# Performance work log

Measured on AMD Instinct MI355X. Metric: run time of the kernel, lower is better.

Reference implementation:

```python
import jax, jax.numpy as jnp
import numpy as np

B, L, DIM, H, D = 2, 2048, 1024, 16, 64


def setup_inputs() -> dict:
    key = jax.random.key(0)
    ks = jax.random.split(key, 20)
    s = 1.0 / np.sqrt(DIM)
    inp = {
        "query": jax.random.normal(ks[0], (B, L, DIM), jnp.float32),
        "keys": jax.random.normal(ks[1], (B, L, DIM), jnp.float32),
        "values": jax.random.normal(ks[2], (B, L, DIM), jnp.float32),
        "focus_vector": jax.random.normal(ks[3], (B, DIM), jnp.float32),
        "temporal_weights": jax.random.normal(ks[4], (B, L), jnp.float32),
        "importance_weights": jax.random.normal(ks[5], (B, L), jnp.float32),
        # linear params, stored [in, out] for x @ W + b
        "Wq": jax.random.normal(ks[6], (DIM, H * D), jnp.float32) * s,
        "bq": jnp.zeros((H * D,), jnp.float32),
        "Wk": jax.random.normal(ks[7], (DIM, H * D), jnp.float32) * s,
        "bk": jnp.zeros((H * D,), jnp.float32),
        "Wv": jax.random.normal(ks[8], (DIM, H * D), jnp.float32) * s,
        "bv": jnp.zeros((H * D,), jnp.float32),
        "Wp": jax.random.normal(ks[9], (H * D, DIM), jnp.float32) * s,
        "bp": jnp.zeros((DIM,), jnp.float32),
        "Wt": jax.random.normal(ks[10], (DIM, 1), jnp.float32) * s,
        "bt": jnp.zeros((1,), jnp.float32),
        "Wi": jax.random.normal(ks[11], (DIM, 1), jnp.float32) * s,
        "bi": jnp.zeros((1,), jnp.float32),
    }
    return inp


def reference(query, keys, values, focus_vector, temporal_weights, importance_weights,
              Wq, bq, Wk, bk, Wv, bv, Wp, bp, Wt, bt, Wi, bi):
    b, l, _ = query.shape
    # QKV projections -> [B, H, L, D]
    q = (query @ Wq + bq).reshape(b, l, H, D).transpose(0, 2, 1, 3)
    k = (keys @ Wk + bk).reshape(b, -1, H, D).transpose(0, 2, 1, 3)
    v = (values @ Wv + bv).reshape(b, -1, H, D).transpose(0, 2, 1, 3)
    scores = jnp.einsum("bhqd,bhkd->bhqk", q, k) / np.sqrt(D).astype(np.float32)
    # gate-modulated weights over keys [B, Lk]
    temporal_scores = (keys @ Wt + bt)[..., 0]
    tw = jax.nn.softmax(temporal_scores * temporal_weights, axis=-1)
    importance_scores = (keys @ Wi + bi)[..., 0]
    iw = jax.nn.softmax(importance_scores * importance_weights, axis=-1)
    rw = jax.nn.softmax(jnp.einsum("bkd,bd->bk", keys, focus_vector), axis=-1)
    combined = (tw + iw + rw) / 3.0
    scores = scores * combined[:, None, None, :]
    weights = jax.nn.softmax(scores, axis=-1)  # dropout is identity in eval
    out = jnp.einsum("bhqk,bhkd->bhqd", weights, v)
    out = out.transpose(0, 2, 1, 3).reshape(b, l, H * D)
    out = out @ Wp + bp
    return out, weights
```

## Files before the change

kernel.cpp:

```cpp
#include <hip/hip_runtime.h>
#include <hip/hip_bf16.h>
#include <cstdint>

#define DEV static __device__ __forceinline__

typedef __attribute__((ext_vector_type(8))) short short8_;
typedef __attribute__((ext_vector_type(4))) float float4_;
typedef __attribute__((ext_vector_type(4))) float f4v;
typedef __attribute__((ext_vector_type(4))) unsigned short u16x4;
typedef __attribute__((ext_vector_type(2))) uint32_t u32x2;
typedef unsigned short u16;

constexpr int Bb   = 2;
constexpr int Ls   = 2048;
constexpr int DIMc = 1024;
constexpr int Hh   = 16;
constexpr int Dd   = 64;
constexpr int BL   = Bb * Ls;
constexpr int HD   = Hh * Dd;

DEV u16 f2bf(float f) {
  union { float f; uint32_t u; } v; v.f = f;
  return (u16)((v.u + 0x7fffu + ((v.u >> 16) & 1u)) >> 16);
}

DEV float4_ mfma16(short8_ a, short8_ b, float4_ c) {
  return __builtin_amdgcn_mfma_f32_16x16x32_bf16(a, b, c, 0, 0, 0);
}

DEV void gload_lds16(const void* g, void* l) {
  __builtin_amdgcn_global_load_lds(
      (const __attribute__((address_space(1))) void*)g,
      (__attribute__((address_space(3))) void*)l, 16, 0, 0);
}

__global__ void k_prep(const float* __restrict__ query, const float* __restrict__ keys,
                       const float* __restrict__ values, u16* __restrict__ qx,
                       u16* __restrict__ kx, u16* __restrict__ vx,
                       const float* __restrict__ Wq, const float* __restrict__ Wk,
                       const float* __restrict__ Wv, const float* __restrict__ Wp,
                       u16* __restrict__ WqT, u16* __restrict__ WkT,
                       u16* __restrict__ WvT, u16* __restrict__ WpT,
                       const float* __restrict__ Wt, const float* __restrict__ bt,
                       const float* __restrict__ Wi, const float* __restrict__ bi,
                       const float* __restrict__ focus,
                       float* __restrict__ ts, float* __restrict__ is_,
                       float* __restrict__ rs) {
  __shared__ float t[64][65];
  const int bid = blockIdx.x, tid = threadIdx.x;
  if (bid < 12288) {
    int z = bid >> 12;
    const float* s = (z == 0) ? query : (z == 1) ? keys : values;
    u16* d = (z == 0) ? qx : (z == 1) ? kx : vx;
    int i = (bid & 4095) * 256 + tid;
    f4v v = ((const f4v*)s)[i];
    u16x4 o = { f2bf(v[0]), f2bf(v[1]), f2bf(v[2]), f2bf(v[3]) };
    ((u16x4*)d)[i] = o;
  } else if (bid < 13312) {
    int r2 = bid - 12288;
    int z = r2 >> 8, rem = r2 & 255;
    const float* W = (z == 0) ? Wq : (z == 1) ? Wk : (z == 2) ? Wv : Wp;
    u16* WT = (z == 0) ? WqT : (z == 1) ? WkT : (z == 2) ? WvT : WpT;
    int n0 = (rem >> 4) * 64, k0 = (rem & 15) * 64;
    int tx = tid & 63, tg = tid >> 6;
#pragma unroll
    for (int i = 0; i < 16; ++i) {
      int r = tg * 16 + i;
      t[r][tx] = W[(size_t)(k0 + r) * HD + n0 + tx];
    }
    __syncthreads();
#pragma unroll
    for (int i = 0; i < 16; ++i) {
      int r = tg * 16 + i;
      WT[(size_t)(n0 + r) * DIMc + k0 + tx] = f2bf(t[tx][r]);
    }
  } else {
    int wv = tid >> 6, ln = tid & 63;
    int row = (bid - 13312) * 4 + wv;
    int b = row >> 11;
    const float* kr = keys + (size_t)row * DIMc;
    const float* fr = focus + (size_t)b * DIMc;
    float st = 0.f, si = 0.f, sr = 0.f;
    for (int j = ln; j < DIMc; j += 64) {
      float kv = kr[j];
      st += kv * Wt[j]; si += kv * Wi[j]; sr += kv * fr[j];
    }
#pragma unroll
    for (int m = 1; m < 64; m <<= 1) {
      st += __shfl_xor(st, m); si += __shfl_xor(si, m); sr += __shfl_xor(sr, m);
    }
    if (ln == 0) { ts[row] = st + bt[0]; is_[row] = si + bi[0]; rs[row] = sr; }
  }
}

__global__ void k_combined(const float* __restrict__ ts, const float* __restrict__ is_,
                           const float* __restrict__ rs, const float* __restrict__ tw,
                           const float* __restrict__ iw, float* __restrict__ comb) {
  int b = blockIdx.x, t = threadIdx.x;
  __shared__ float red[3][4];
  float lt[8], li[8], lr[8];
  float m3[3] = {-1e30f, -1e30f, -1e30f};
#pragma unroll
  for (int i = 0; i < 8; ++i) {
    int gi = b * Ls + i * 256 + t;
    lt[i] = ts[gi] * tw[gi];
    li[i] = is_[gi] * iw[gi];
    lr[i] = rs[gi];
    m3[0] = fmaxf(m3[0], lt[i]); m3[1] = fmaxf(m3[1], li[i]); m3[2] = fmaxf(m3[2], lr[i]);
  }
#pragma unroll
  for (int q = 0; q < 3; ++q) {
    float v = m3[q];
#pragma unroll
    for (int m = 32; m; m >>= 1) v = fmaxf(v, __shfl_xor(v, m));
    if ((t & 63) == 0) red[q][t >> 6] = v;
  }
  __syncthreads();
#pragma unroll
  for (int q = 0; q < 3; ++q)
    m3[q] = fmaxf(fmaxf(red[q][0], red[q][1]), fmaxf(red[q][2], red[q][3]));
  __syncthreads();
  float s3[3] = {0.f, 0.f, 0.f};
#pragma unroll
  for (int i = 0; i < 8; ++i) {
    lt[i] = __expf(lt[i] - m3[0]); s3[0] += lt[i];
    li[i] = __expf(li[i] - m3[1]); s3[1] += li[i];
    lr[i] = __expf(lr[i] - m3[2]); s3[2] += lr[i];
  }
#pragma unroll
  for (int q = 0; q < 3; ++q) {
    float v = s3[q];
#pragma unroll
    for (int m = 32; m; m >>= 1) v += __shfl_xor(v, m);
    if ((t & 63) == 0) red[q][t >> 6] = v;
  }
  __syncthreads();
#pragma unroll
  for (int q = 0; q < 3; ++q) s3[q] = red[q][0] + red[q][1] + red[q][2] + red[q][3];
  float rt = 1.f / s3[0], ri = 1.f / s3[1], rr = 1.f / s3[2];
  const float scl = (1.f / 3.f) * 0.125f;
#pragma unroll
  for (int i = 0; i < 8; ++i) {
    int gi = b * Ls + i * 256 + t;
    comb[gi] = (lt[i] * rt + li[i] * ri + lr[i] * rr) * scl;
  }
}

__launch_bounds__(256, 2)
__global__ void k_gemm_qkv(const u16* __restrict__ qx, const u16* __restrict__ kx,
                           const u16* __restrict__ vx, const u16* __restrict__ WqT,
                           const u16* __restrict__ WkT, const u16* __restrict__ WvT,
                           const float* __restrict__ bq, const float* __restrict__ bk,
                           const float* __restrict__ bv, u16* __restrict__ q_bh,
                           u16* __restrict__ k_bh, u16* __restrict__ vT) {
  __shared__ __align__(16) u16 As[128 * 32];
  __shared__ __align__(16) u16 Bs[128 * 32];
  const int z = blockIdx.z;
  const u16* A  = (z == 0) ? qx : (z == 1) ? kx : vx;
  const u16* BT = (z == 0) ? WqT : (z == 1) ? WkT : WvT;
  const float* bias = (z == 0) ? bq : (z == 1) ? bk : bv;
  const int tid = threadIdx.x, wv = tid >> 6, ln = tid & 63;
  const int g = ln >> 4, c = ln & 15;
  const int m0 = blockIdx.x * 128, n0 = blockIdx.y * 128;
  const int wm = wv >> 1, wn = wv & 1;
  const float4_ z4 = {0.f, 0.f, 0.f, 0.f};
  float4_ acc[4][4];
#pragma unroll
  for (int i = 0; i < 4; ++i)
#pragma unroll
    for (int j = 0; j < 4; ++j) acc[i][j] = z4;
  const int lrow = ln >> 2, lcol = (ln & 3) * 8;
  for (int k0 = 0; k0 < 1024; k0 += 32) {
#pragma unroll
    for (int s = 0; s < 2; ++s) {
      int r0 = wv * 32 + s * 16;
      gload_lds16(A  + (size_t)(m0 + r0 + lrow) * 1024 + k0 + lcol, &As[r0 * 32]);
      gload_lds16(BT + (size_t)(n0 + r0 + lrow) * 1024 + k0 + lcol, &Bs[r0 * 32]);
    }
    __syncthreads();
    short8_ af[4], bfr[4];
#pragma unroll
    for (int mt = 0; mt < 4; ++mt)
      af[mt] = *(const short8_*)&As[(wm * 64 + mt * 16 + c) * 32 + g * 8];
#pragma unroll
    for (int nt = 0; nt < 4; ++nt)
      bfr[nt] = *(const short8_*)&Bs[(wn * 64 + nt * 16 + c) * 32 + g * 8];
#pragma unroll
    for (int mt = 0; mt < 4; ++mt)
#pragma unroll
      for (int nt = 0; nt < 4; ++nt)
        acc[mt][nt] = mfma16(af[mt], bfr[nt], acc[mt][nt]);
    __syncthreads();
  }
  if (z < 2) {
    u16* Q = (z == 0) ? q_bh : k_bh;
#pragma unroll
    for (int mt = 0; mt < 4; ++mt)
#pragma unroll
      for (int nt = 0; nt < 4; ++nt) {
        int n = n0 + wn * 64 + nt * 16 + c;
        float bv_ = bias[n];
        int h = n >> 6, d = n & 63;
#pragma unroll
        for (int r = 0; r < 4; ++r) {
          int m = m0 + wm * 64 + mt * 16 + g * 4 + r;
          int b = m >> 11, l = m & 2047;
          Q[((size_t)((b * Hh + h) * Ls + l)) * Dd + d] = f2bf(acc[mt][nt][r] + bv_);
        }
      }
  } else {
#pragma unroll
    for (int mt = 0; mt < 4; ++mt)
#pragma unroll
      for (int nt = 0; nt < 4; ++nt) {
        int n = n0 + wn * 64 + nt * 16 + c;
        float bv_ = bias[n];
        int h = n >> 6, d = n & 63;
        int mrow = m0 + wm * 64 + mt * 16 + g * 4;
        int b = mrow >> 11, l = mrow & 2047;
        u16x4 o = { f2bf(acc[mt][nt][0] + bv_), f2bf(acc[mt][nt][1] + bv_),
                    f2bf(acc[mt][nt][2] + bv_), f2bf(acc[mt][nt][3] + bv_) };
        *(u16x4*)&vT[((size_t)((b * Hh + h) * Dd + d)) * Ls + l] = o;
      }
  }
}

__launch_bounds__(256, 4)
__global__ void k_attn_p1(const u16* __restrict__ q_bh, const u16* __restrict__ k_bh,
                          const u16* __restrict__ vT, const float* __restrict__ comb_g,
                          u16* __restrict__ ctx, float* __restrict__ inv_g) {
  __shared__ __align__(16) u16 Kt[2][64][64];
  __shared__ __align__(16) u16 Vt[2][64][64];
  __shared__ __align__(16) uint32_t Ew[4][16][32];

  const int bid = blockIdx.x;
  const int logical = (bid & 7) * 128 + (bid >> 3);
  const int bh = logical >> 5, qb = logical & 31;
  const int b = bh >> 4, h = bh & 15;
  const int l0 = qb * 64;
  const int w = threadIdx.x >> 6, ln = threadIdx.x & 63;
  const int g = ln >> 4, c = ln & 15;
  const int srow = ln >> 3, x8 = ln & 7;
  const float4_ z4 = {0.f, 0.f, 0.f, 0.f};

  const u16* kbh = k_bh + (size_t)bh * Ls * Dd;
  const u16* vbh = vT + (size_t)bh * Dd * Ls;
  const float* kcomb = comb_g + (size_t)b * Ls;

  const u16* qp = q_bh + ((size_t)bh * Ls + l0 + w * 16) * Dd;
  short8_ aq0 = *(const short8_*)&qp[c * Dd + g * 8];
  short8_ aq1 = *(const short8_*)&qp[c * Dd + 32 + g * 8];

  auto stageK = [&](int buf, int kb) {
#pragma unroll
    for (int i = 0; i < 2; ++i) {
      int rr = w * 16 + i * 8 + srow;
      int sc = (x8 ^ (rr & 7)) * 8;
      gload_lds16(kbh + (size_t)(kb + rr) * Dd + sc, &Kt[buf][w * 16 + i * 8][0]);
    }
  };
  auto stageV = [&](int buf, int kb) {
#pragma unroll
    for (int i = 0; i < 2; ++i) {
      int rr = w * 16 + i * 8 + srow;
      int sc = (x8 ^ (rr & 7)) * 8;
      gload_lds16(vbh + (size_t)rr * Ls + kb + sc, &Vt[buf][w * 16 + i * 8][0]);
    }
  };

  float4_ accO[4];
#pragma unroll
  for (int dt = 0; dt < 4; ++dt) accO[dt] = z4;
  float rs_loc = 0.f;

  stageK(0, 0); stageV(0, 0);
  __syncthreads();

  int buf = 0;
  for (int t = 0; t < 32; ++t) {
    if (t < 31) { stageK(buf ^ 1, (t + 1) * 64); stageV(buf ^ 1, (t + 1) * 64); }
    const int kb = t * 64;
#pragma unroll
    for (int s = 0; s < 4; ++s) {
      int rowK = s * 16 + c;
      short8_ bk0 = *(const short8_*)&Kt[buf][rowK][((g    ) ^ (c & 7)) * 8];
      short8_ bk1 = *(const short8_*)&Kt[buf][rowK][((4 + g) ^ (c & 7)) * 8];
      float4_ st = mfma16(bk0, aq0, z4);
      st = mfma16(bk1, aq1, st);
      float4_ cc4 = *(const float4_*)&kcomb[kb + s * 16 + g * 4];
      float e0 = __expf(st[0] * cc4[0]);
      float e1 = __expf(st[1] * cc4[1]);
      float e2 = __expf(st[2] * cc4[2]);
      float e3 = __expf(st[3] * cc4[3]);
      rs_loc += (e0 + e1) + (e2 + e3);
      uint32_t lo = ((uint32_t)f2bf(e1) << 16) | f2bf(e0);
      uint32_t hi = ((uint32_t)f2bf(e3) << 16) | f2bf(e2);
      int chunk = (s * 2 + (g >> 1)) ^ (c & 7);
      u32x2 pk = { lo, hi };
      *(u32x2*)&Ew[w][c][chunk * 4 + (g & 1) * 2] = pk;
    }
#pragma unroll
    for (int hf = 0; hf < 2; ++hf) {
      short8_ ea = *(const short8_*)&Ew[w][c][((hf * 4 + g) ^ (c & 7)) * 4];
#pragma unroll
      for (int dt = 0; dt < 4; ++dt) {
        short8_ bv = *(const short8_*)&Vt[buf][dt * 16 + c][((hf * 4 + g) ^ (c & 7)) * 8];
        accO[dt] = mfma16(ea, bv, accO[dt]);
      }
    }
    __syncthreads();
    buf ^= 1;
  }

  rs_loc += __shfl_xor(rs_loc, 16);
  rs_loc += __shfl_xor(rs_loc, 32);
  float inv = 1.0f / rs_loc;
  if (ln < 16) inv_g[(size_t)bh * Ls + l0 + w * 16 + ln] = inv;
  float invrow[4];
#pragma unroll
  for (int r = 0; r < 4; ++r) invrow[r] = __shfl(inv, g * 4 + r);

  u16* out_lds = &Vt[0][0][0] + w * 1152;
#pragma unroll
  for (int dt = 0; dt < 4; ++dt)
#pragma unroll
    for (int r = 0; r < 4; ++r)
      out_lds[(g * 4 + r) * 72 + dt * 16 + c] = f2bf(accO[dt][r] * invrow[r]);
  {
    int rr2 = ln >> 2, sg = ln & 3;
    short8_ d0 = *(const short8_*)&out_lds[rr2 * 72 + sg * 16];
    short8_ d1 = *(const short8_*)&out_lds[rr2 * 72 + sg * 16 + 8];
    u16* cp = ctx + ((size_t)(b * Ls + l0 + w * 16 + rr2)) * HD + h * Dd + sg * 16;
    *(short8_*)cp = d0;
    *(short8_*)(cp + 8) = d1;
  }
}

__launch_bounds__(256, 4)
__global__ void k_p2(const u16* __restrict__ ctx, const u16* __restrict__ WpT,
                     const float* __restrict__ bp, float* __restrict__ O,
                     const u16* __restrict__ q_bh, const u16* __restrict__ k_bh,
                     const float* __restrict__ comb_g, const float* __restrict__ inv_g,
                     float* __restrict__ wout) {
  __shared__ __align__(16) char smem[2 * 64 * 64 * 2];
  const int tid = threadIdx.x, wv = tid >> 6, ln = tid & 63;
  const int g = ln >> 4, c = ln & 15;
  const float4_ z4 = {0.f, 0.f, 0.f, 0.f};

  if (blockIdx.x < 512) {
    u16* As = (u16*)smem;
    u16* Bs = (u16*)(smem + 4096);
    const int m0 = (int)(blockIdx.x >> 3) * 64, n0 = (int)(blockIdx.x & 7) * 128;
    const int wm = wv >> 1, wn = wv & 1;
    float4_ acc[2][4];
#pragma unroll
    for (int i = 0; i < 2; ++i)
#pragma unroll
      for (int j = 0; j < 4; ++j) acc[i][j] = z4;
    const int lrow = ln >> 2, lcol = (ln & 3) * 8;
    for (int k0 = 0; k0 < 1024; k0 += 32) {
      gload_lds16(ctx + (size_t)(m0 + wv * 16 + lrow) * 1024 + k0 + lcol, &As[(wv * 16) * 32]);
#pragma unroll
      for (int s = 0; s < 2; ++s) {
        int r0 = wv * 32 + s * 16;
        gload_lds16(WpT + (size_t)(n0 + r0 + lrow) * 1024 + k0 + lcol, &Bs[r0 * 32]);
      }
      __syncthreads();
      short8_ af[2], bfr[4];
#pragma unroll
      for (int mt = 0; mt < 2; ++mt)
        af[mt] = *(const short8_*)&As[(wm * 32 + mt * 16 + c) * 32 + g * 8];
#pragma unroll
      for (int nt = 0; nt < 4; ++nt)
        bfr[nt] = *(const short8_*)&Bs[(wn * 64 + nt * 16 + c) * 32 + g * 8];
#pragma unroll
      for (int mt = 0; mt < 2; ++mt)
#pragma unroll
        for (int nt = 0; nt < 4; ++nt)
          acc[mt][nt] = mfma16(af[mt], bfr[nt], acc[mt][nt]);
      __syncthreads();
    }
#pragma unroll
    for (int mt = 0; mt < 2; ++mt)
#pragma unroll
      for (int nt = 0; nt < 4; ++nt) {
        int n = n0 + wn * 64 + nt * 16 + c;
        float bv_ = bp[n];
#pragma unroll
        for (int r = 0; r < 4; ++r) {
          int m = m0 + wm * 32 + mt * 16 + g * 4 + r;
          O[(size_t)m * HD + n] = acc[mt][nt][r] + bv_;
        }
      }
  } else {
    typedef u16 (*KtT)[64][64];
    KtT Kt = (KtT)smem;
    const int abid = blockIdx.x - 512;
    const int logical = (abid & 7) * 128 + (abid >> 3);
    const int bh = logical >> 5, qb = logical & 31;
    const int b = bh >> 4;
    const int l0 = qb * 64;
    const int srow = ln >> 3, x8 = ln & 7;
    const u16* kbh = k_bh + (size_t)bh * Ls * Dd;
    const float* kcomb = comb_g + (size_t)b * Ls;
    const u16* qp = q_bh + ((size_t)bh * Ls + l0 + wv * 16) * Dd;
    short8_ aq0 = *(const short8_*)&qp[c * Dd + g * 8];
    short8_ aq1 = *(const short8_*)&qp[c * Dd + 32 + g * 8];
    float ivq = inv_g[(size_t)bh * Ls + l0 + wv * 16 + c];

    auto stageK = [&](int buf, int kb) {
#pragma unroll
      for (int i = 0; i < 2; ++i) {
        int rr = wv * 16 + i * 8 + srow;
        int sc = (x8 ^ (rr & 7)) * 8;
        gload_lds16(kbh + (size_t)(kb + rr) * Dd + sc, &Kt[buf][wv * 16 + i * 8][0]);
      }
    };
    stageK(0, 0);
    __syncthreads();
    int buf = 0;
    float* wb = wout + ((size_t)bh * Ls + l0 + wv * 16) * Ls;
    for (int t = 0; t < 32; ++t) {
      if (t < 31) stageK(buf ^ 1, (t + 1) * 64);
      const int kb = t * 64;
#pragma unroll
      for (int s = 0; s < 4; ++s) {
        int rowK = s * 16 + c;
        short8_ bk0 = *(const short8_*)&Kt[buf][rowK][((g    ) ^ (c & 7)) * 8];
        short8_ bk1 = *(const short8_*)&Kt[buf][rowK][((4 + g) ^ (c & 7)) * 8];
        float4_ st = mfma16(bk0, aq0, z4);
        st = mfma16(bk1, aq1, st);
        float4_ cc4 = *(const float4_*)&kcomb[kb + s * 16 + g * 4];
        float4_ o;
#pragma unroll
        for (int r = 0; r < 4; ++r) o[r] = __expf(st[r] * cc4[r]) * ivq;
        __builtin_nontemporal_store(o, (float4_*)&wb[(size_t)c * Ls + kb + s * 16 + g * 4]);
      }
      __syncthreads();
      buf ^= 1;
    }
  }
}

extern "C" void kernel_launch(void* const* d_in, const int* in_sizes, int n_in,
                              void* d_out, int out_size, void* d_ws, size_t ws_size,
                              hipStream_t stream) {
  (void)in_sizes; (void)n_in; (void)out_size; (void)ws_size;
  const float* query = (const float*)d_in[0];
  const float* keys  = (const float*)d_in[1];
  const float* values= (const float*)d_in[2];
  const float* focus = (const float*)d_in[3];
  const float* twg   = (const float*)d_in[4];
  const float* iwg   = (const float*)d_in[5];
  const float* Wq = (const float*)d_in[6];  const float* bq = (const float*)d_in[7];
  const float* Wk = (const float*)d_in[8];  const float* bk = (const float*)d_in[9];
  const float* Wv = (const float*)d_in[10]; const float* bv = (const float*)d_in[11];
  const float* Wp = (const float*)d_in[12]; const float* bp = (const float*)d_in[13];
  const float* Wt = (const float*)d_in[14]; const float* bt = (const float*)d_in[15];
  const float* Wi = (const float*)d_in[16]; const float* bi = (const float*)d_in[17];

  char* ws = (char*)d_ws;
  size_t off = 0;
  auto alloc = [&](size_t bytes) -> char* {
    char* p = ws + off; off += (bytes + 255) & ~(size_t)255; return p;
  };
  const size_t NTOK = (size_t)BL * DIMc;
  u16* qx   = (u16*)alloc(NTOK * 2);
  u16* kx   = (u16*)alloc(NTOK * 2);
  u16* vx   = (u16*)alloc(NTOK * 2);
  u16* WqT  = (u16*)alloc((size_t)DIMc * HD * 2);
  u16* WkT  = (u16*)alloc((size_t)DIMc * HD * 2);
  u16* WvT  = (u16*)alloc((size_t)DIMc * HD * 2);
  u16* WpT  = (u16*)alloc((size_t)DIMc * HD * 2);
  u16* q_bh = (u16*)alloc(NTOK * 2);
  u16* k_bh = (u16*)alloc(NTOK * 2);
  u16* vTb  = (u16*)alloc(NTOK * 2);
  u16* ctx  = (u16*)alloc(NTOK * 2);
  float* ts   = (float*)alloc((size_t)BL * 4);
  float* is_  = (float*)alloc((size_t)BL * 4);
  float* rs   = (float*)alloc((size_t)BL * 4);
  float* comb = (float*)alloc((size_t)BL * 4);
  float* invg = (float*)alloc((size_t)BL * 16 * 4);

  float* out_f = (float*)d_out;
  float* w_out = out_f + (size_t)BL * HD;

  k_prep<<<14336, 256, 0, stream>>>(query, keys, values, qx, kx, vx,
                                    Wq, Wk, Wv, Wp, WqT, WkT, WvT, WpT,
                                    Wt, bt, Wi, bi, focus, ts, is_, rs);
  k_combined<<<2, 256, 0, stream>>>(ts, is_, rs, twg, iwg, comb);
  dim3 gq(32, 8, 3);
  k_gemm_qkv<<<gq, 256, 0, stream>>>(qx, kx, vx, WqT, WkT, WvT, bq, bk, bv,
                                     q_bh, k_bh, vTb);
  k_attn_p1<<<1024, 256, 0, stream>>>(q_bh, k_bh, vTb, comb, ctx, invg);
  k_p2<<<1536, 256, 0, stream>>>(ctx, WpT, bp, out_f,
                                 q_bh, k_bh, comb, invg, w_out);
}
```

Baseline: 319.2 us.

## Fuse weight-matrix recompute into attention kernel and split out-projection GEMM

The attention kernel now writes the normalized softmax weights itself in a second pass over K right after computing the context, instead of storing per-row inverse sums and recomputing scores in a combined projection/weights kernel. The output projection becomes a standalone GEMM kernel. This removes the inv_g round trip and the heterogeneous co-scheduled kernel, but serializes the 64 MB weight write inside the attention kernel and drops the nontemporal store hint. QKV GEMM launch bounds are also raised to 3 blocks per CU.

Result: faster. 293.6 us (-8.0%).

```diff
diff --git a/kernel.cpp b/kernel.cpp
--- a/kernel.cpp
+++ b/kernel.cpp
@@ -146,7 +146,7 @@
   }
 }
 
-__launch_bounds__(256, 2)
+__launch_bounds__(256, 3)
 __global__ void k_gemm_qkv(const u16* __restrict__ qx, const u16* __restrict__ kx,
                            const u16* __restrict__ vx, const u16* __restrict__ WqT,
                            const u16* __restrict__ WkT, const u16* __restrict__ WvT,
@@ -226,9 +226,9 @@
 }
 
 __launch_bounds__(256, 4)
-__global__ void k_attn_p1(const u16* __restrict__ q_bh, const u16* __restrict__ k_bh,
-                          const u16* __restrict__ vT, const float* __restrict__ comb_g,
-                          u16* __restrict__ ctx, float* __restrict__ inv_g) {
+__global__ void k_attn4(const u16* __restrict__ q_bh, const u16* __restrict__ k_bh,
+                        const u16* __restrict__ vT, const float* __restrict__ comb_g,
+                        float* __restrict__ wout, u16* __restrict__ ctx) {
   __shared__ __align__(16) u16 Kt[2][64][64];
   __shared__ __align__(16) u16 Vt[2][64][64];
   __shared__ __align__(16) uint32_t Ew[4][16][32];
@@ -315,7 +315,6 @@
   rs_loc += __shfl_xor(rs_loc, 16);
   rs_loc += __shfl_xor(rs_loc, 32);
   float inv = 1.0f / rs_loc;
-  if (ln < 16) inv_g[(size_t)bh * Ls + l0 + w * 16 + ln] = inv;
   float invrow[4];
 #pragma unroll
   for (int r = 0; r < 4; ++r) invrow[r] = __shfl(inv, g * 4 + r);
@@ -334,112 +333,82 @@
     *(short8_*)cp = d0;
     *(short8_*)(cp + 8) = d1;
   }
+
+  stageK(0, 0);
+  __syncthreads();
+  buf = 0;
+  float* wb = wout + ((size_t)bh * Ls + l0 + w * 16) * Ls;
+  for (int t = 0; t < 32; ++t) {
+    if (t < 31) stageK(buf ^ 1, (t + 1) * 64);
+    const int kb = t * 64;
+#pragma unroll
+    for (int s = 0; s < 4; ++s) {
+      int rowK = s * 16 + c;
+      short8_ bk0 = *(const short8_*)&Kt[buf][rowK][((g    ) ^ (c & 7)) * 8];
+      short8_ bk1 = *(const short8_*)&Kt[buf][rowK][((4 + g) ^ (c & 7)) * 8];
+      float4_ st = mfma16(bk0, aq0, z4);
+      st = mfma16(bk1, aq1, st);
+      float4_ cc4 = *(const float4_*)&kcomb[kb + s * 16 + g * 4];
+      float4_ o;
+#pragma unroll
+      for (int r = 0; r < 4; ++r) o[r] = __expf(st[r] * cc4[r]) * inv;
+      *(float4_*)&wb[(size_t)c * Ls + kb + s * 16 + g * 4] = o;
+    }
+    __syncthreads();
+    buf ^= 1;
+  }
 }
 
 __launch_bounds__(256, 4)
-__global__ void k_p2(const u16* __restrict__ ctx, const u16* __restrict__ WpT,
-                     const float* __restrict__ bp, float* __restrict__ O,
-                     const u16* __restrict__ q_bh, const u16* __restrict__ k_bh,
-                     const float* __restrict__ comb_g, const float* __restrict__ inv_g,
-                     float* __restrict__ wout) {
-  __shared__ __align__(16) char smem[2 * 64 * 64 * 2];
+__global__ void k_gemmO(const u16* __restrict__ A, const u16* __restrict__ BT,
+                        const float* __restrict__ bias, float* __restrict__ O) {
+  __shared__ __align__(16) u16 As[64 * 32];
+  __shared__ __align__(16) u16 Bs[128 * 32];
   const int tid = threadIdx.x, wv = tid >> 6, ln = tid & 63;
   const int g = ln >> 4, c = ln & 15;
+  const int m0 = blockIdx.x * 64, n0 = blockIdx.y * 128;
+  const int wm = wv >> 1, wn = wv & 1;
   const float4_ z4 = {0.f, 0.f, 0.f, 0.f};
-
-  if (blockIdx.x < 512) {
-    u16* As = (u16*)smem;
-    u16* Bs = (u16*)(smem + 4096);
-    const int m0 = (int)(blockIdx.x >> 3) * 64, n0 = (int)(blockIdx.x & 7) * 128;
-    const int wm = wv >> 1, wn = wv & 1;
-    float4_ acc[2][4];
-#pragma unroll
-    for (int i = 0; i < 2; ++i)
-#pragma unroll
-      for (int j = 0; j < 4; ++j) acc[i][j] = z4;
-    const int lrow = ln >> 2, lcol = (ln & 3) * 8;
-    for (int k0 = 0; k0 < 1024; k0 += 32) {
-      gload_lds16(ctx + (size_t)(m0 + wv * 16 + lrow) * 1024 + k0 + lcol, &As[(wv * 16) * 32]);
-#pragma unroll
-      for (int s = 0; s < 2; ++s) {
-        int r0 = wv * 32 + s * 16;
-        gload_lds16(WpT + (size_t)(n0 + r0 + lrow) * 1024 + k0 + lcol, &Bs[r0 * 32]);
+  float4_ acc[2][4];
+#pragma unroll
+  for (int i = 0; i < 2; ++i)
+#pragma unroll
+    for (int j = 0; j < 4; ++j) acc[i][j] = z4;
+  const int lrow = ln >> 2, lcol = (ln & 3) * 8;
+  for (int k0 = 0; k0 < 1024; k0 += 32) {
+    gload_lds16(A + (size_t)(m0 + wv * 16 + lrow) * 1024 + k0 + lcol, &As[(wv * 16) * 32]);
+#pragma unroll
+    for (int s = 0; s < 2; ++s) {
+      int r0 = wv * 32 + s * 16;
+      gload_lds16(BT + (size_t)(n0 + r0 + lrow) * 1024 + k0 + lcol, &Bs[r0 * 32]);
+    }
+    __syncthreads();
+    short8_ af[2], bfr[4];
+#pragma unroll
+    for (int mt = 0; mt < 2; ++mt)
+      af[mt] = *(const short8_*)&As[(wm * 32 + mt * 16 + c) * 32 + g * 8];
+#pragma unroll
+    for (int nt = 0; nt < 4; ++nt)
+      bfr[nt] = *(const short8_*)&Bs[(wn * 64 + nt * 16 + c) * 32 + g * 8];
+#pragma unroll
+    for (int mt = 0; mt < 2; ++mt)
+#pragma unroll
+      for (int nt = 0; nt < 4; ++nt)
+        acc[mt][nt] = mfma16(af[mt], bfr[nt], acc[mt][nt]);
+    __syncthreads();
+  }
+#pragma unroll
+  for (int mt = 0; mt < 2; ++mt)
+#pragma unroll
+    for (int nt = 0; nt < 4; ++nt) {
+      int n = n0 + wn * 64 + nt * 16 + c;
+      float bv_ = bias[n];
+#pragma unroll
+      for (int r = 0; r < 4; ++r) {
+        int m = m0 + wm * 32 + mt * 16 + g * 4 + r;
+        O[(size_t)m * HD + n] = acc[mt][nt][r] + bv_;
       }
-      __syncthreads();
-      short8_ af[2], bfr[4];
-#pragma unroll
-      for (int mt = 0; mt < 2; ++mt)
-        af[mt] = *(const short8_*)&As[(wm * 32 + mt * 16 + c) * 32 + g * 8];
-#pragma unroll
-      for (int nt = 0; nt < 4; ++nt)
-        bfr[nt] = *(const short8_*)&Bs[(wn * 64 + nt * 16 + c) * 32 + g * 8];
-#pragma unroll
-      for (int mt = 0; mt < 2; ++mt)
-#pragma unroll
-        for (int nt = 0; nt < 4; ++nt)
-          acc[mt][nt] = mfma16(af[mt], bfr[nt], acc[mt][nt]);
-      __syncthreads();
-    }
-#pragma unroll
-    for (int mt = 0; mt < 2; ++mt)
-#pragma unroll
-      for (int nt = 0; nt < 4; ++nt) {
-        int n = n0 + wn * 64 + nt * 16 + c;
-        float bv_ = bp[n];
-#pragma unroll
-        for (int r = 0; r < 4; ++r) {
-          int m = m0 + wm * 32 + mt * 16 + g * 4 + r;
-          O[(size_t)m * HD + n] = acc[mt][nt][r] + bv_;
-        }
-      }
-  } else {
-    typedef u16 (*KtT)[64][64];
-    KtT Kt = (KtT)smem;
-    const int abid = blockIdx.x - 512;
-    const int logical = (abid & 7) * 128 + (abid >> 3);
-    const int bh = logical >> 5, qb = logical & 31;
-    const int b = bh >> 4;
-    const int l0 = qb * 64;
-    const int srow = ln >> 3, x8 = ln & 7;
-    const u16* kbh = k_bh + (size_t)bh * Ls * Dd;
-    const float* kcomb = comb_g + (size_t)b * Ls;
-    const u16* qp = q_bh + ((size_t)bh * Ls + l0 + wv * 16) * Dd;
-    short8_ aq0 = *(const short8_*)&qp[c * Dd + g * 8];
-    short8_ aq1 = *(const short8_*)&qp[c * Dd + 32 + g * 8];
-    float ivq = inv_g[(size_t)bh * Ls + l0 + wv * 16 + c];
-
-    auto stageK = [&](int buf, int kb) {
-#pragma unroll
-      for (int i = 0; i < 2; ++i) {
-        int rr = wv * 16 + i * 8 + srow;
-        int sc = (x8 ^ (rr & 7)) * 8;
-        gload_lds16(kbh + (size_t)(kb + rr) * Dd + sc, &Kt[buf][wv * 16 + i * 8][0]);
-      }
-    };
-    stageK(0, 0);
-    __syncthreads();
-    int buf = 0;
-    float* wb = wout + ((size_t)bh * Ls + l0 + wv * 16) * Ls;
-    for (int t = 0; t < 32; ++t) {
-      if (t < 31) stageK(buf ^ 1, (t + 1) * 64);
-      const int kb = t * 64;
-#pragma unroll
-      for (int s = 0; s < 4; ++s) {
-        int rowK = s * 16 + c;
-        short8_ bk0 = *(const short8_*)&Kt[buf][rowK][((g    ) ^ (c & 7)) * 8];
-        short8_ bk1 = *(const short8_*)&Kt[buf][rowK][((4 + g) ^ (c & 7)) * 8];
-        float4_ st = mfma16(bk0, aq0, z4);
-        st = mfma16(bk1, aq1, st);
-        float4_ cc4 = *(const float4_*)&kcomb[kb + s * 16 + g * 4];
-        float4_ o;
-#pragma unroll
-        for (int r = 0; r < 4; ++r) o[r] = __expf(st[r] * cc4[r]) * ivq;
-        __builtin_nontemporal_store(o, (float4_*)&wb[(size_t)c * Ls + kb + s * 16 + g * 4]);
-      }
-      __syncthreads();
-      buf ^= 1;
-    }
-  }
+    }
 }
 
 extern "C" void kernel_launch(void* const* d_in, const int* in_sizes, int n_in,
@@ -480,7 +449,6 @@
   float* is_  = (float*)alloc((size_t)BL * 4);
   float* rs   = (float*)alloc((size_t)BL * 4);
   float* comb = (float*)alloc((size_t)BL * 4);
-  float* invg = (float*)alloc((size_t)BL * 16 * 4);
 
   float* out_f = (float*)d_out;
   float* w_out = out_f + (size_t)BL * HD;
@@ -492,7 +460,7 @@
   dim3 gq(32, 8, 3);
   k_gemm_qkv<<<gq, 256, 0, stream>>>(qx, kx, vx, WqT, WkT, WvT, bq, bk, bv,
                                      q_bh, k_bh, vTb);
-  k_attn_p1<<<1024, 256, 0, stream>>>(q_bh, k_bh, vTb, comb, ctx, invg);
-  k_p2<<<1536, 256, 0, stream>>>(ctx, WpT, bp, out_f,
-                                 q_bh, k_bh, comb, invg, w_out);
-}
+  k_attn4<<<1024, 256, 0, stream>>>(q_bh, k_bh, vTb, comb, w_out, ctx);
+  dim3 go(64, 8);
+  k_gemmO<<<go, 256, 0, stream>>>(ctx, WpT, bp, out_f);
+}
```
